# Kernel optimization log

Measured on AMD Instinct MI355X. Metric: run time of the kernel, lower is better.

Reference implementation:

```python
import jax, jax.numpy as jnp
import numpy as np

DIM = 2048
N_HEADS = 16
N_KV_HEADS = 4
HEAD_DIM = DIM // N_HEADS  # 128
T = 2048


def setup_inputs() -> dict:
    key = jax.random.key(0)
    k1, k2, k3 = jax.random.split(key, 3)
    scale = 1.0 / np.sqrt(DIM)
    x = jax.random.normal(k1, (T, DIM), dtype=jnp.float32)
    # GQA-consistent fused QKV projection: q (n_h*hd) + k (n_kv*hd) + v (n_kv*hd)
    qkv_out = (N_HEADS + 2 * N_KV_HEADS) * HEAD_DIM  # 3072
    W_qkv = jax.random.normal(k2, (DIM, qkv_out), dtype=jnp.float32) * scale
    W_o = jax.random.normal(k3, (N_HEADS * HEAD_DIM, DIM), dtype=jnp.float32) * scale
    return {"x": x, "W_qkv": W_qkv, "W_o": W_o}


def reference(x, W_qkv, W_o):
    Tn, C = x.shape
    hd = HEAD_DIM
    qkv = x @ W_qkv  # [T, (n_h + 2*n_kv)*hd]
    q, k, v = jnp.split(qkv, [N_HEADS * hd, (N_HEADS + N_KV_HEADS) * hd], axis=-1)
    q = q.reshape(Tn, N_HEADS, hd).transpose(1, 0, 2)      # [n_h, T, hd]
    k = k.reshape(Tn, N_KV_HEADS, hd).transpose(1, 0, 2)   # [n_kv, T, hd]
    v = v.reshape(Tn, N_KV_HEADS, hd).transpose(1, 0, 2)
    rep = N_HEADS // N_KV_HEADS
    k = jnp.repeat(k, rep, axis=0)  # [n_h, T, hd]
    v = jnp.repeat(v, rep, axis=0)
    scores = jnp.einsum('hid,hjd->hij', q, k) / jnp.sqrt(jnp.asarray(hd, x.dtype))
    causal = jnp.tril(jnp.ones((Tn, Tn), dtype=bool))[None, :, :]
    scores = jnp.where(causal, scores, -jnp.inf)
    attn = jax.nn.softmax(scores, axis=-1)
    out = jnp.einsum('hij,hjd->hid', attn, v)  # [n_h, T, hd]
    out = out.transpose(1, 0, 2).reshape(Tn, N_HEADS * hd)
    return out @ W_o
```

## Files before the change

### kernel.cpp

```cpp
#include <hip/hip_runtime.h>
#include <stdint.h>

#define T_SEQ   2048
#define DMODEL  2048
#define NH      16
#define HD      128
#define QKVN    3072
#define KCOL    2048
#define VCOL    2560

typedef __bf16 bf16x8 __attribute__((ext_vector_type(8)));
typedef float  f32x4  __attribute__((ext_vector_type(4)));
typedef unsigned short u16x8 __attribute__((ext_vector_type(8)));

__device__ __forceinline__ uint16_t f2bf(float f) {
    uint32_t u = __builtin_bit_cast(uint32_t, f);
    u += 0x7fffu + ((u >> 16) & 1u);
    return (uint16_t)(u >> 16);
}
__device__ __forceinline__ float bf2f(uint16_t u) {
    return __builtin_bit_cast(float, (uint32_t)u << 16);
}
__device__ __forceinline__ u16x8 ld8(const uint16_t* p) {
    return *reinterpret_cast<const u16x8*>(p);
}
__device__ __forceinline__ void st8(uint16_t* p, u16x8 v) {
    *reinterpret_cast<u16x8*>(p) = v;
}
__device__ __forceinline__ bf16x8 as_bf(u16x8 v) { return __builtin_bit_cast(bf16x8, v); }

__device__ __forceinline__ uint32_t cvtpk(float a, float b) {
    uint32_t r;
    asm("v_cvt_pk_bf16_f32 %0, %1, %2" : "=v"(r) : "v"(a), "v"(b));
    return r;
}

__device__ __forceinline__ void gl_lds16(const uint16_t* g, uint16_t* l) {
    __builtin_amdgcn_global_load_lds((const __attribute__((address_space(1))) void*)g,
                                     (__attribute__((address_space(3))) void*)l, 16, 0, 0);
}

__global__ __launch_bounds__(256) void k_cast(const float* __restrict__ in,
                                              uint16_t* __restrict__ out, int n8) {
    int i = blockIdx.x * 256 + threadIdx.x;
    if (i >= n8) return;
    const f32x4* p = reinterpret_cast<const f32x4*>(in) + (size_t)i * 2;
    f32x4 a = p[0], b = p[1];
    u16x8 o;
    o[0] = f2bf(a[0]); o[1] = f2bf(a[1]); o[2] = f2bf(a[2]); o[3] = f2bf(a[3]);
    o[4] = f2bf(b[0]); o[5] = f2bf(b[1]); o[6] = f2bf(b[2]); o[7] = f2bf(b[3]);
    reinterpret_cast<u16x8*>(out)[i] = o;
}

__global__ __launch_bounds__(256) void k_tcast(const float* __restrict__ in,
                                               uint16_t* __restrict__ out, int R, int C) {
    __shared__ uint16_t tile[64][72];
    int t = threadIdx.x;
    int rbase = blockIdx.y * 64, cbase = blockIdx.x * 64;
#pragma unroll
    for (int p = 0; p < 4; ++p) {
        int ir = p * 16 + (t >> 4);
        int ic = (t & 15) * 4;
        f32x4 v = *reinterpret_cast<const f32x4*>(&in[(size_t)(rbase + ir) * C + cbase + ic]);
        tile[ir][ic + 0] = f2bf(v[0]);
        tile[ir][ic + 1] = f2bf(v[1]);
        tile[ir][ic + 2] = f2bf(v[2]);
        tile[ir][ic + 3] = f2bf(v[3]);
    }
    __syncthreads();
#pragma unroll
    for (int p = 0; p < 2; ++p) {
        int oc = p * 32 + (t >> 3);
        int orr = (t & 7) * 8;
        u16x8 o;
#pragma unroll
        for (int e = 0; e < 8; ++e) o[e] = tile[orr + e][oc];
        st8(&out[(size_t)(cbase + oc) * R + rbase + orr], o);
    }
}

__global__ __launch_bounds__(256) void k_tbf16(const uint16_t* __restrict__ in,
                                               uint16_t* __restrict__ out,
                                               int R, int C, int ldin, int coff) {
    __shared__ uint16_t tile[64][72];
    int t = threadIdx.x;
    int rbase = blockIdx.y * 64, cbase = blockIdx.x * 64;
#pragma unroll
    for (int p = 0; p < 2; ++p) {
        int ir = p * 32 + (t >> 3);
        int ic = (t & 7) * 8;
        u16x8 v = ld8(&in[(size_t)(rbase + ir) * ldin + coff + cbase + ic]);
#pragma unroll
        for (int e = 0; e < 8; ++e) tile[ir][ic + e] = v[e];
    }
    __syncthreads();
#pragma unroll
    for (int p = 0; p < 2; ++p) {
        int oc = p * 32 + (t >> 3);
        int orr = (t & 7) * 8;
        u16x8 o;
#pragma unroll
        for (int e = 0; e < 8; ++e) o[e] = tile[orr + e][oc];
        st8(&out[(size_t)(cbase + oc) * R + rbase + orr], o);
    }
}

__global__ __launch_bounds__(256) void k_gemm(const uint16_t* __restrict__ A,
                                              const uint16_t* __restrict__ Bt,
                                              void* __restrict__ Cout,
                                              int M, int N, int K, int gy,
                                              int out_bf16, int scale_cols, float qscale) {
    __shared__ __align__(16) uint16_t Asm[2][64 * 64];
    __shared__ __align__(16) uint16_t Bsm[2][128 * 64];
    int t = threadIdx.x;
    int w = t >> 6, lane = t & 63, lo = lane & 15, g4 = lane >> 4;

    int nwg = (int)gridDim.x;
    int wg = (int)blockIdx.x;
    int idx = (wg & 7) * (nwg >> 3) + (wg >> 3);
    int bx = idx / gy, by = idx % gy;
    int mbase = by * 64, nbase = bx * 128;

    int wm = w >> 1, wn = w & 1;

    const uint16_t* pA[2]; int lofsA[2];
#pragma unroll
    for (int c = 0; c < 2; ++c) {
        int ch = w * 2 + c;
        int r = ch * 8 + (lane >> 3);
        pA[c] = A + (size_t)(mbase + r) * K + (((lane & 7) ^ (r & 7)) * 8);
        lofsA[c] = ch * 512;
    }
    const uint16_t* pB[4]; int lofsB[4];
#pragma unroll
    for (int c = 0; c < 4; ++c) {
        int ch = w * 4 + c;
        int r = ch * 8 + (lane >> 3);
        pB[c] = Bt + (size_t)(nbase + r) * K + (((lane & 7) ^ (r & 7)) * 8);
        lofsB[c] = ch * 512;
    }

    f32x4 acc[2][4] = {};

#pragma unroll
    for (int c = 0; c < 2; ++c) gl_lds16(pA[c], &Asm[0][lofsA[c]]);
#pragma unroll
    for (int c = 0; c < 4; ++c) gl_lds16(pB[c], &Bsm[0][lofsB[c]]);

    int cur = 0;
    for (int kt = 0; kt < K; kt += 64) {
        __syncthreads();
        if (kt + 64 < K) {
            int ko = kt + 64;
#pragma unroll
            for (int c = 0; c < 2; ++c) gl_lds16(pA[c] + ko, &Asm[cur ^ 1][lofsA[c]]);
#pragma unroll
            for (int c = 0; c < 4; ++c) gl_lds16(pB[c] + ko, &Bsm[cur ^ 1][lofsB[c]]);
        }
        bf16x8 af[2][2], bfr[2][4];
#pragma unroll
        for (int ks = 0; ks < 2; ++ks) {
#pragma unroll
            for (int i = 0; i < 2; ++i) {
                int ar = wm * 32 + i * 16 + lo;
                af[ks][i] = as_bf(ld8(&Asm[cur][(ar * 64 + ks * 32 + g4 * 8) ^ ((lo & 7) << 3)]));
            }
#pragma unroll
            for (int j = 0; j < 4; ++j) {
                int br = wn * 64 + j * 16 + lo;
                bfr[ks][j] = as_bf(ld8(&Bsm[cur][(br * 64 + ks * 32 + g4 * 8) ^ ((lo & 7) << 3)]));
            }
        }
        __builtin_amdgcn_s_setprio(1);
#pragma unroll
        for (int ks = 0; ks < 2; ++ks)
#pragma unroll
            for (int i = 0; i < 2; ++i)
#pragma unroll
                for (int j = 0; j < 4; ++j)
                    acc[i][j] = __builtin_amdgcn_mfma_f32_16x16x32_bf16(af[ks][i], bfr[ks][j], acc[i][j], 0, 0, 0);
        __builtin_amdgcn_s_setprio(0);
        cur ^= 1;
    }

    if (out_bf16) {
        uint16_t* C = (uint16_t*)Cout;
#pragma unroll
        for (int i = 0; i < 2; ++i)
#pragma unroll
            for (int j = 0; j < 4; ++j)
#pragma unroll
                for (int r = 0; r < 4; ++r) {
                    int row = mbase + wm * 32 + i * 16 + g4 * 4 + r;
                    int col = nbase + wn * 64 + j * 16 + lo;
                    float v = acc[i][j][r];
                    if (col < scale_cols) v *= qscale;
                    C[(size_t)row * N + col] = f2bf(v);
                }
    } else {
        float* C = (float*)Cout;
#pragma unroll
        for (int i = 0; i < 2; ++i)
#pragma unroll
            for (int j = 0; j < 4; ++j)
#pragma unroll
                for (int r = 0; r < 4; ++r) {
                    int row = mbase + wm * 32 + i * 16 + g4 * 4 + r;
                    int col = nbase + wn * 64 + j * 16 + lo;
                    C[(size_t)row * N + col] = acc[i][j][r];
                }
    }
}

__global__ __launch_bounds__(256) void k_attn(const uint16_t* __restrict__ qkv,
                                              const uint16_t* __restrict__ vt,
                                              uint16_t* __restrict__ po,
                                              float* __restrict__ pml) {
    __shared__ __align__(16) uint16_t Ksm[2][64 * 128];
    __shared__ __align__(16) uint16_t Vsm[2][128 * 64];
    __shared__ __align__(16) uint16_t Psm[4][16 * 72];
    int t = threadIdx.x;
    int w = t >> 6, lane = t & 63, lo = lane & 15, g4 = lane >> 4;
    int x = blockIdx.x, h = blockIdx.y, p = blockIdx.z, kh = h >> 2;

    const uint16_t* kbase = qkv + KCOL + (size_t)kh * HD;
    const uint16_t* vbase = vt + (size_t)(kh * HD) * T_SEQ;

    const uint16_t* kp[4]; const uint16_t* vp[4]; int lofs[4];
#pragma unroll
    for (int c = 0; c < 4; ++c) {
        int ch = w * 4 + c;
        int kr = ch * 4 + (lane >> 4);
        kp[c] = kbase + (size_t)kr * QKVN + ((lane & 15) ^ (kr & 7)) * 8;
        int vr = ch * 8 + (lane >> 3);
        vp[c] = vbase + (size_t)vr * T_SEQ + ((lane & 7) ^ (vr & 7)) * 8;
        lofs[c] = ch * 512;
    }

    for (int rep = 0; rep < 2; ++rep) {
        int qt = rep ? 31 - x : x;
        int qb = qt * 64;
        int cnt = (qt + 2 - p) >> 1;

        bf16x8 qf[4];
        {
            int qrow = qb + w * 16 + lo;
            const uint16_t* qp = &qkv[(size_t)qrow * QKVN + h * HD + g4 * 8];
#pragma unroll
            for (int ks = 0; ks < 4; ++ks) qf[ks] = as_bf(ld8(qp + ks * 32));
        }

        f32x4 o[8] = {};
        float mr = -INFINITY, pp = 0.f;

        if (cnt) {
            __syncthreads();
            size_t ko = (size_t)p * 64 * QKVN; int vo = p * 64;
#pragma unroll
            for (int c = 0; c < 4; ++c) {
                gl_lds16(kp[c] + ko, &Ksm[0][lofs[c]]);
                gl_lds16(vp[c] + vo, &Vsm[0][lofs[c]]);
            }
        }

        int cur = 0;
        for (int it = 0; it < cnt; ++it) {
            int jt = p + 2 * it;
            __syncthreads();
            if (it + 1 < cnt) {
                size_t ko = (size_t)(jt + 2) * 64 * QKVN;
                int vo = (jt + 2) * 64;
#pragma unroll
                for (int c = 0; c < 4; ++c) {
                    gl_lds16(kp[c] + ko, &Ksm[cur ^ 1][lofs[c]]);
                    gl_lds16(vp[c] + vo, &Vsm[cur ^ 1][lofs[c]]);
                }
            }

            f32x4 s[4] = {};
            __builtin_amdgcn_s_setprio(1);
#pragma unroll
            for (int nt = 0; nt < 4; ++nt) {
                int j = nt * 16 + lo;
#pragma unroll
                for (int ks = 0; ks < 4; ++ks) {
                    bf16x8 a = as_bf(ld8(&Ksm[cur][(j * 128 + ks * 32 + g4 * 8) ^ ((lo & 7) << 3)]));
                    s[nt] = __builtin_amdgcn_mfma_f32_16x16x32_bf16(a, qf[ks], s[nt], 0, 0, 0);
                }
            }
            __builtin_amdgcn_s_setprio(0);

            if (jt == qt) {
                int i = qb + w * 16 + lo;
                int jb = jt * 64;
#pragma unroll
                for (int nt = 0; nt < 4; ++nt)
#pragma unroll
                    for (int r = 0; r < 4; ++r) {
                        int j = jb + nt * 16 + g4 * 4 + r;
                        if (j > i) s[nt][r] = -INFINITY;
                    }
            }

            float pm = fmaxf(
                fmaxf(fmaxf(fmaxf(s[0][0], s[0][1]), fmaxf(s[0][2], s[0][3])),
                      fmaxf(fmaxf(s[1][0], s[1][1]), fmaxf(s[1][2], s[1][3]))),
                fmaxf(fmaxf(fmaxf(s[2][0], s[2][1]), fmaxf(s[2][2], s[2][3])),
                      fmaxf(fmaxf(s[3][0], s[3][1]), fmaxf(s[3][2], s[3][3]))));
            pm = fmaxf(pm, __shfl_xor(pm, 16));
            pm = fmaxf(pm, __shfl_xor(pm, 32));

            if (__any(pm > mr + 11.f)) {
                float mn = fmaxf(mr, pm);
                float al = exp2f(fminf(fmaxf(mr, -1e30f) - mn, 0.f));
                mr = mn;
                pp *= al;
                float alo[4];
#pragma unroll
                for (int r = 0; r < 4; ++r)
                    alo[r] = __shfl(al, (lane & 48) | (((lane >> 4) << 2) + r));
#pragma unroll
                for (int dt = 0; dt < 8; ++dt)
#pragma unroll
                    for (int r = 0; r < 4; ++r) o[dt][r] *= alo[r];
            }
            float msafe = fmaxf(mr, -1e30f);
#pragma unroll
            for (int nt = 0; nt < 4; ++nt)
#pragma unroll
                for (int r = 0; r < 4; ++r) {
                    float pe = exp2f(s[nt][r] - msafe);
                    s[nt][r] = pe;
                    pp += pe;
                }
#pragma unroll
            for (int nt = 0; nt < 4; ++nt) {
                uint32_t p01 = cvtpk(s[nt][0], s[nt][1]);
                uint32_t p23 = cvtpk(s[nt][2], s[nt][3]);
                *reinterpret_cast<uint2*>(&Psm[w][lo * 72 + nt * 16 + g4 * 4]) =
                    make_uint2(p01, p23);
            }

            __builtin_amdgcn_s_setprio(1);
#pragma unroll
            for (int ks2 = 0; ks2 < 2; ++ks2) {
                bf16x8 pa = as_bf(ld8(&Psm[w][lo * 72 + ks2 * 32 + g4 * 8]));
#pragma unroll
                for (int dt = 0; dt < 8; ++dt) {
                    int d = dt * 16 + lo;
                    bf16x8 vb = as_bf(ld8(&Vsm[cur][(d * 64 + ks2 * 32 + g4 * 8) ^ ((lo & 7) << 3)]));
                    o[dt] = __builtin_amdgcn_mfma_f32_16x16x32_bf16(pa, vb, o[dt], 0, 0, 0);
                }
            }
            __builtin_amdgcn_s_setprio(0);
            cur ^= 1;
        }

        float lr = pp;
        lr += __shfl_xor(lr, 16);
        lr += __shfl_xor(lr, 32);

        uint16_t* pob = po + (size_t)p * T_SEQ * DMODEL;
#pragma unroll
        for (int dt = 0; dt < 8; ++dt)
#pragma unroll
            for (int r = 0; r < 4; ++r) {
                int i = qb + w * 16 + g4 * 4 + r;
                int col = h * HD + dt * 16 + lo;
                pob[(size_t)i * DMODEL + col] = f2bf(o[dt][r]);
            }
        if (lane < 16) {
            int i = qb + w * 16 + lane;
            float* pe = pml + (size_t)p * T_SEQ * NH * 2 + ((size_t)i * NH + h) * 2;
            pe[0] = mr;
            pe[1] = lr;
        }
    }
}

__global__ __launch_bounds__(256) void k_comb(uint16_t* __restrict__ po,
                                              const float* __restrict__ pml) {
    int i = blockIdx.x * 256 + threadIdx.x;
    int row = i >> 8;
    int cg = i & 255;
    int h = cg >> 4;
    int col = cg * 8;
    const size_t PS = (size_t)T_SEQ * NH * 2;
    const size_t TD = (size_t)T_SEQ * DMODEL;
    size_t mo = ((size_t)row * NH + h) * 2;
    float m0 = pml[mo], l0 = pml[mo + 1];
    float m1 = pml[PS + mo], l1 = pml[PS + mo + 1];
    float m = fmaxf(m0, m1);
    float w0 = exp2f(m0 - m), w1 = exp2f(m1 - m);
    float rl = 1.f / (l0 * w0 + l1 * w1);
    size_t off = (size_t)row * DMODEL + col;
    u16x8 a = ld8(po + off);
    u16x8 b = ld8(po + TD + off);
    u16x8 o;
#pragma unroll
    for (int e = 0; e < 8; ++e)
        o[e] = f2bf((bf2f(a[e]) * w0 + bf2f(b[e]) * w1) * rl);
    st8(po + off, o);
}

extern "C" void kernel_launch(void* const* d_in, const int* in_sizes, int n_in,
                              void* d_out, int out_size, void* d_ws, size_t ws_size,
                              hipStream_t stream) {
    (void)in_sizes; (void)n_in; (void)out_size; (void)ws_size;
    const float* x    = (const float*)d_in[0];
    const float* Wqkv = (const float*)d_in[1];
    const float* Wo   = (const float*)d_in[2];
    float* out = (float*)d_out;

    char* ws = (char*)d_ws;
    uint16_t* xb   = (uint16_t*)(ws + 0);
    uint16_t* wqt  = (uint16_t*)(ws + 8388608);
    uint16_t* po   = (uint16_t*)(ws + 0);
    float*    pml  = (float*)(ws + 16777216);
    uint16_t* wot  = (uint16_t*)(ws + 20971520);
    uint16_t* qkvb = (uint16_t*)(ws + 29360128);
    uint16_t* vtb  = (uint16_t*)(ws + 41943040);

    const float qscale = 0.12751743f;

    k_cast<<<2048, 256, 0, stream>>>(x, xb, 524288);
    k_tcast<<<dim3(48, 32), 256, 0, stream>>>(Wqkv, wqt, 2048, 3072);
    k_tcast<<<dim3(32, 32), 256, 0, stream>>>(Wo, wot, 2048, 2048);
    k_gemm<<<768, 256, 0, stream>>>(xb, wqt, qkvb, 2048, 3072, 2048, 32, 1, 2048, qscale);
    k_tbf16<<<dim3(8, 32), 256, 0, stream>>>(qkvb, vtb, 2048, 512, 3072, 2560);
    k_attn<<<dim3(16, 16, 2), 256, 0, stream>>>(qkvb, vtb, po, pml);
    k_comb<<<2048, 256, 0, stream>>>(po, pml);
    k_gemm<<<512, 256, 0, stream>>>(po, wot, out, 2048, 2048, 2048, 32, 0, 0, 1.0f);
}
```

Baseline: 133.7 us.

## Split attention KV range three ways and read V directly from global

The attention kernel now splits the key range across three partitions instead of two, launching 1.5x more blocks, and the combine kernel merges three partial results. V tiles are no longer staged in shared memory. Each lane loads its V fragment straight from the transposed V buffer in global memory, which cuts LDS use and allows a launch bound of three blocks per CU. The risk is more global and cache traffic for V, plus a larger partial-output workspace and combine cost.

```diff
diff --git a/kernel.cpp b/kernel.cpp
--- a/kernel.cpp
+++ b/kernel.cpp
@@ -212,35 +212,32 @@
     }
 }
 
-__global__ __launch_bounds__(256) void k_attn(const uint16_t* __restrict__ qkv,
-                                              const uint16_t* __restrict__ vt,
-                                              uint16_t* __restrict__ po,
-                                              float* __restrict__ pml) {
+__global__ __launch_bounds__(256, 3) void k_attn(const uint16_t* __restrict__ qkv,
+                                                 const uint16_t* __restrict__ vt,
+                                                 uint16_t* __restrict__ po,
+                                                 float* __restrict__ pml) {
     __shared__ __align__(16) uint16_t Ksm[2][64 * 128];
-    __shared__ __align__(16) uint16_t Vsm[2][128 * 64];
     __shared__ __align__(16) uint16_t Psm[4][16 * 72];
     int t = threadIdx.x;
     int w = t >> 6, lane = t & 63, lo = lane & 15, g4 = lane >> 4;
     int x = blockIdx.x, h = blockIdx.y, p = blockIdx.z, kh = h >> 2;
 
     const uint16_t* kbase = qkv + KCOL + (size_t)kh * HD;
-    const uint16_t* vbase = vt + (size_t)(kh * HD) * T_SEQ;
-
-    const uint16_t* kp[4]; const uint16_t* vp[4]; int lofs[4];
+    const uint16_t* vlane = vt + ((size_t)(kh * HD) + lo) * T_SEQ + g4 * 8;
+
+    const uint16_t* kp[4]; int lofs[4];
 #pragma unroll
     for (int c = 0; c < 4; ++c) {
         int ch = w * 4 + c;
         int kr = ch * 4 + (lane >> 4);
         kp[c] = kbase + (size_t)kr * QKVN + ((lane & 15) ^ (kr & 7)) * 8;
-        int vr = ch * 8 + (lane >> 3);
-        vp[c] = vbase + (size_t)vr * T_SEQ + ((lane & 7) ^ (vr & 7)) * 8;
         lofs[c] = ch * 512;
     }
 
     for (int rep = 0; rep < 2; ++rep) {
         int qt = rep ? 31 - x : x;
         int qb = qt * 64;
-        int cnt = (qt + 2 - p) >> 1;
+        int cnt = (qt + 3 - p) / 3;
 
         bf16x8 qf[4];
         {
@@ -255,26 +252,19 @@
 
         if (cnt) {
             __syncthreads();
-            size_t ko = (size_t)p * 64 * QKVN; int vo = p * 64;
-#pragma unroll
-            for (int c = 0; c < 4; ++c) {
-                gl_lds16(kp[c] + ko, &Ksm[0][lofs[c]]);
-                gl_lds16(vp[c] + vo, &Vsm[0][lofs[c]]);
-            }
+            size_t ko = (size_t)p * 64 * QKVN;
+#pragma unroll
+            for (int c = 0; c < 4; ++c) gl_lds16(kp[c] + ko, &Ksm[0][lofs[c]]);
         }
 
         int cur = 0;
         for (int it = 0; it < cnt; ++it) {
-            int jt = p + 2 * it;
+            int jt = p + 3 * it;
             __syncthreads();
             if (it + 1 < cnt) {
-                size_t ko = (size_t)(jt + 2) * 64 * QKVN;
-                int vo = (jt + 2) * 64;
-#pragma unroll
-                for (int c = 0; c < 4; ++c) {
-                    gl_lds16(kp[c] + ko, &Ksm[cur ^ 1][lofs[c]]);
-                    gl_lds16(vp[c] + vo, &Vsm[cur ^ 1][lofs[c]]);
-                }
+                size_t ko = (size_t)(jt + 3) * 64 * QKVN;
+#pragma unroll
+                for (int c = 0; c < 4; ++c) gl_lds16(kp[c] + ko, &Ksm[cur ^ 1][lofs[c]]);
             }
 
             f32x4 s[4] = {};
@@ -344,11 +334,11 @@
             __builtin_amdgcn_s_setprio(1);
 #pragma unroll
             for (int ks2 = 0; ks2 < 2; ++ks2) {
+                const uint16_t* vjt = vlane + jt * 64 + ks2 * 32;
                 bf16x8 pa = as_bf(ld8(&Psm[w][lo * 72 + ks2 * 32 + g4 * 8]));
 #pragma unroll
                 for (int dt = 0; dt < 8; ++dt) {
-                    int d = dt * 16 + lo;
-                    bf16x8 vb = as_bf(ld8(&Vsm[cur][(d * 64 + ks2 * 32 + g4 * 8) ^ ((lo & 7) << 3)]));
+                    bf16x8 vb = as_bf(ld8(vjt + (size_t)(dt * 16) * T_SEQ));
                     o[dt] = __builtin_amdgcn_mfma_f32_16x16x32_bf16(pa, vb, o[dt], 0, 0, 0);
                 }
             }
@@ -388,18 +378,20 @@
     const size_t PS = (size_t)T_SEQ * NH * 2;
     const size_t TD = (size_t)T_SEQ * DMODEL;
     size_t mo = ((size_t)row * NH + h) * 2;
-    float m0 = pml[mo], l0 = pml[mo + 1];
-    float m1 = pml[PS + mo], l1 = pml[PS + mo + 1];
-    float m = fmaxf(m0, m1);
-    float w0 = exp2f(m0 - m), w1 = exp2f(m1 - m);
-    float rl = 1.f / (l0 * w0 + l1 * w1);
+    float m0 = pml[mo],          l0 = pml[mo + 1];
+    float m1 = pml[PS + mo],     l1 = pml[PS + mo + 1];
+    float m2 = pml[2 * PS + mo], l2 = pml[2 * PS + mo + 1];
+    float m = fmaxf(fmaxf(m0, m1), m2);
+    float w0 = exp2f(m0 - m), w1 = exp2f(m1 - m), w2 = exp2f(m2 - m);
+    float rl = 1.f / (l0 * w0 + l1 * w1 + l2 * w2);
     size_t off = (size_t)row * DMODEL + col;
     u16x8 a = ld8(po + off);
     u16x8 b = ld8(po + TD + off);
+    u16x8 c = ld8(po + 2 * TD + off);
     u16x8 o;
 #pragma unroll
     for (int e = 0; e < 8; ++e)
-        o[e] = f2bf((bf2f(a[e]) * w0 + bf2f(b[e]) * w1) * rl);
+        o[e] = f2bf((bf2f(a[e]) * w0 + bf2f(b[e]) * w1 + bf2f(c[e]) * w2) * rl);
     st8(po + off, o);
 }
 
@@ -416,10 +408,10 @@
     uint16_t* xb   = (uint16_t*)(ws + 0);
     uint16_t* wqt  = (uint16_t*)(ws + 8388608);
     uint16_t* po   = (uint16_t*)(ws + 0);
-    float*    pml  = (float*)(ws + 16777216);
-    uint16_t* wot  = (uint16_t*)(ws + 20971520);
-    uint16_t* qkvb = (uint16_t*)(ws + 29360128);
-    uint16_t* vtb  = (uint16_t*)(ws + 41943040);
+    float*    pml  = (float*)(ws + 25165824);
+    uint16_t* wot  = (uint16_t*)(ws + 25952256);
+    uint16_t* qkvb = (uint16_t*)(ws + 34340864);
+    uint16_t* vtb  = (uint16_t*)(ws + 46923776);
 
     const float qscale = 0.12751743f;
 
@@ -428,7 +420,7 @@
     k_tcast<<<dim3(32, 32), 256, 0, stream>>>(Wo, wot, 2048, 2048);
     k_gemm<<<768, 256, 0, stream>>>(xb, wqt, qkvb, 2048, 3072, 2048, 32, 1, 2048, qscale);
     k_tbf16<<<dim3(8, 32), 256, 0, stream>>>(qkvb, vtb, 2048, 512, 3072, 2560);
-    k_attn<<<dim3(16, 16, 2), 256, 0, stream>>>(qkvb, vtb, po, pml);
+    k_attn<<<dim3(16, 16, 3), 256, 0, stream>>>(qkvb, vtb, po, pml);
     k_comb<<<2048, 256, 0, stream>>>(po, pml);
     k_gemm<<<512, 256, 0, stream>>>(po, wot, out, 2048, 2048, 2048, 32, 0, 0, 1.0f);
 }
```

Result: slower. 171.9 us (+28.6%).
